# Performance work log

Measured on AMD Instinct MI355X. Metric: run time of the kernel, lower is better.

Reference implementation:

```python
import jax, jax.numpy as jnp
import numpy as np

N = 100_000      # nodes
E = 3_200_000    # edges
F_IN = 9
F_HID = 9
F_OUT = 1
EPS = 1e-5

def _ln(x, g, b):
    m = x.mean(-1, keepdims=True)
    v = x.var(-1, keepdims=True)
    return (x - m) / jnp.sqrt(v + EPS) * g + b

def _gat(x, src, dst, edge_attr, W, a_src, a_dst, We, a_e, bias):
    # Single-head GATConv with edge_dim=1, add_self_loops=True, fill_value='mean'
    n = x.shape[0]
    loop = jnp.arange(n)
    deg = jax.ops.segment_sum(jnp.ones((src.shape[0],), x.dtype), dst, n)
    loop_attr = jax.ops.segment_sum(edge_attr, dst, n) / jnp.maximum(deg, 1.0)[:, None]
    s = jnp.concatenate([src, loop])
    d = jnp.concatenate([dst, loop])
    ea = jnp.concatenate([edge_attr, loop_attr], axis=0)   # [E+N, 1]
    xp = x @ W                                             # [N, C]
    a = (xp * a_src).sum(-1)[s] + (xp * a_dst).sum(-1)[d] + ((ea @ We) * a_e).sum(-1)
    a = jax.nn.leaky_relu(a, 0.2)
    amax = jax.ops.segment_max(a, d, n)
    aexp = jnp.exp(a - amax[d])
    denom = jax.ops.segment_sum(aexp, d, n)
    alpha = aexp / (denom[d] + 1e-16)
    return jax.ops.segment_sum(alpha[:, None] * xp[s], d, n) + bias

def setup_inputs() -> dict:
    key = jax.random.key(0)
    ks = jax.random.split(key, 16)
    def rn(k, shp, s):
        return jax.random.normal(k, shp, jnp.float32) * s
    return {
        "x": jax.random.normal(ks[0], (N, F_IN), jnp.float32),
        "edge_index": jax.random.randint(ks[1], (2, E), 0, N, jnp.int32),
        "edge_attr": jax.random.normal(ks[2], (E, 1), jnp.float32),
        "ln1_g": jnp.ones((F_IN,), jnp.float32), "ln1_b": jnp.zeros((F_IN,), jnp.float32),
        "W0": rn(ks[3], (F_IN, F_HID), 0.3), "as0": rn(ks[4], (F_HID,), 0.3),
        "ad0": rn(ks[5], (F_HID,), 0.3), "We0": rn(ks[6], (1, F_HID), 0.3),
        "ae0": rn(ks[7], (F_HID,), 0.3), "b0": jnp.zeros((F_HID,), jnp.float32),
        "W1": rn(ks[8], (F_HID, F_HID), 0.3), "as1": rn(ks[9], (F_HID,), 0.3),
        "ad1": rn(ks[10], (F_HID,), 0.3), "We1": rn(ks[11], (1, F_HID), 0.3),
        "ae1": rn(ks[12], (F_HID,), 0.3), "b1": jnp.zeros((F_HID,), jnp.float32),
        "ng1": jnp.ones((F_HID,), jnp.float32), "nb1": jnp.zeros((F_HID,), jnp.float32),
        "ln2_g": jnp.ones((2 * F_HID,), jnp.float32), "ln2_b": jnp.zeros((2 * F_HID,), jnp.float32),
        "et_W": rn(ks[13], (2 * F_HID, F_HID), 0.2), "et_b": jnp.zeros((F_HID,), jnp.float32),
        "fc_W": rn(ks[14], (F_HID, F_OUT), 0.3), "fc_b": jnp.zeros((F_OUT,), jnp.float32),
        "att_W": rn(ks[15], (2 * F_OUT, F_OUT), 0.5), "att_b": jnp.zeros((F_OUT,), jnp.float32),
    }

def reference(x, edge_index, edge_attr, ln1_g, ln1_b, W0, as0, ad0, We0, ae0, b0,
              W1, as1, ad1, We1, ae1, b1, ng1, nb1, ln2_g, ln2_b,
              et_W, et_b, fc_W, fc_b, att_W, att_b):
    src, dst = edge_index[0], edge_index[1]
    h = _ln(x, ln1_g, ln1_b)
    # layer 0: no norm/residual
    h = jax.nn.leaky_relu(_gat(h, src, dst, edge_attr, W0, as0, ad0, We0, ae0, b0), 0.01)
    # layer 1: norm + residual
    ident = h
    h = _ln(_gat(h, src, dst, edge_attr, W1, as1, ad1, We1, ae1, b1), ng1, nb1) + ident
    h = jax.nn.leaky_relu(h, 0.01)
    # edge path: gather-concat-norm-MLP  [E, 2H]
    ef = _ln(jnp.concatenate([h[src], h[dst]], axis=1), ln2_g, ln2_b)
    eo = jax.nn.leaky_relu(ef @ et_W + et_b, 0.01)
    eo = eo @ fc_W + fc_b                       # [E, 1]
    # AttentionLayer
    comb = jnp.concatenate([eo, edge_attr], axis=1)   # [E, 2]
    w = jax.nn.softmax(comb @ att_W + att_b, axis=-1) # [E, 1]
    att = (w * comb).sum(axis=1, keepdims=True)       # [E, 1]
    return att + eo
```

## Files before the change

### kernel.cpp

```cpp
#include <hip/hip_runtime.h>
#include <hip/hip_bf16.h>
#include <hip/hip_fp16.h>

typedef __hip_bfloat16 bf16;
typedef unsigned int uint;
typedef unsigned short ushort;
#define TPB 256
#define TPBS 1024
#define TPBG 1024
#define BSH 7
#define BNODES 128
#define NBK_MAX 1024
#define CH 8192
#define EPT (CH / TPBS)
#define NW (TPBS / 64)
#define GPAD 16
#define CAP 4608

enum {
  LN1G = 0, LN1B = 9, PW0 = 18, AS0 = 99, AD0 = 108, CE0 = 117, B0 = 118,
  PW1 = 127, AS1 = 208, AD1 = 217, CE1 = 226, B1 = 227, NG = 236, NB = 245,
  LN2G = 254, LN2B = 272, ETW = 290, ETB = 452, FCW = 461, FCB = 470,
  GC = 471, KC = 480, ETH = 490, NPARAM = 580
};

#ifdef __has_builtin
#if __has_builtin(__builtin_amdgcn_fdot2)
#define HAVE_FDOT2 1
#endif
#endif
#ifndef HAVE_FDOT2
#define HAVE_FDOT2 0
#endif

typedef _Float16 h2f __attribute__((ext_vector_type(2)));

static __device__ __forceinline__ float lrelu(float x, float s) { return x >= 0.f ? x : s * x; }
static __device__ __forceinline__ float ldx(const void* p, long i, int isb) {
    return isb ? __bfloat162float(((const bf16*)p)[i]) : ((const float*)p)[i];
}
static __device__ __forceinline__ uint bfb(float f) {
    uint u = __float_as_uint(f);
    return (u + 0x7FFFu + ((u >> 16) & 1u)) >> 16;
}
static __device__ __forceinline__ uint pack2(float a, float b) { return bfb(a) | (bfb(b) << 16); }
static __device__ __forceinline__ float unlo(uint u) { return __uint_as_float(u << 16); }
static __device__ __forceinline__ float unhi(uint u) { return __uint_as_float(u & 0xFFFF0000u); }
static __device__ __forceinline__ ushort h16(float f) { return __half_as_ushort(__float2half(f)); }
static __device__ __forceinline__ uint p2h(float a, float b) { return (uint)h16(a) | ((uint)h16(b) << 16); }
static __device__ __forceinline__ float hfl(uint u) { return __half2float(__ushort_as_half((ushort)(u & 0xFFFFu))); }
static __device__ __forceinline__ float hfh(uint u) { return __half2float(__ushort_as_half((ushort)(u >> 16))); }
static __device__ __forceinline__ h2f as_h2(uint u) { union { uint u; h2f h; } x; x.u = u; return x.h; }
static __device__ __forceinline__ float dot2f(uint a, uint w, float acc) {
#if HAVE_FDOT2
    return __builtin_amdgcn_fdot2(as_h2(a), as_h2(w), acc, false);
#else
    return fmaf(hfl(a), hfl(w), fmaf(hfh(a), hfh(w), acc));
#endif
}

__global__ void k_params(const void* ln1g, const void* ln1b,
                         const void* W0, const void* as0, const void* ad0,
                         const void* We0, const void* ae0, const void* b0,
                         const void* W1, const void* as1, const void* ad1,
                         const void* We1, const void* ae1, const void* b1,
                         const void* ng, const void* nb,
                         const void* ln2g, const void* ln2b,
                         const void* etW, const void* etb,
                         const void* fcW, const void* fcb,
                         float* __restrict__ P, int* __restrict__ flagp,
                         int* __restrict__ gcursor, int nbk)
{
    __shared__ int sflag;
    if (threadIdx.x == 0) {
        unsigned short h0 = ((const unsigned short*)ln1g)[0];
        sflag = (h0 == 0x3F80u) ? 1 : 0;
        *flagp = sflag;
    }
    __syncthreads();
    const int f = sflag;
    const int t = threadIdx.x;
    for (int j = t; j < nbk; j += TPB) gcursor[j * GPAD] = j * CAP;
    for (int i = t; i < 9; i += TPB) {
        P[LN1G + i] = ldx(ln1g, i, f); P[LN1B + i] = ldx(ln1b, i, f);
        P[AS0 + i] = ldx(as0, i, f);   P[AD0 + i] = ldx(ad0, i, f);
        P[B0 + i]  = ldx(b0, i, f);
        P[AS1 + i] = ldx(as1, i, f);   P[AD1 + i] = ldx(ad1, i, f);
        P[B1 + i]  = ldx(b1, i, f);
        P[NG + i]  = ldx(ng, i, f);    P[NB + i]  = ldx(nb, i, f);
        P[ETB + i] = ldx(etb, i, f);   P[FCW + i] = ldx(fcW, i, f);
    }
    for (int i = t; i < 81; i += TPB) { P[PW0 + i] = ldx(W0, i, f); P[PW1 + i] = ldx(W1, i, f); }
    for (int i = t; i < 18; i += TPB) { P[LN2G + i] = ldx(ln2g, i, f); P[LN2B + i] = ldx(ln2b, i, f); }
    for (int i = t; i < 162; i += TPB) P[ETW + i] = ldx(etW, i, f) * ldx(ln2g, i / 9, f);
    __syncthreads();
    for (int i = t; i < 90; i += TPB) {
        int role = i / 45, rem = i % 45, c = rem / 5, p = rem % 5;
        int k0 = 2 * p, k1 = 2 * p + 1;
        float w0 = (k0 < 9) ? P[ETW + (role * 9 + k0) * 9 + c] : 0.f;
        float w1 = (k1 < 9) ? P[ETW + (role * 9 + k1) * 9 + c] : 0.f;
        ((uint*)P)[ETH + i] = p2h(w0, w1);
    }
    if (t == 0) {
        float c0 = 0.f, c1 = 0.f;
        for (int k = 0; k < 9; k++) {
            c0 += ldx(We0, k, f) * ldx(ae0, k, f);
            c1 += ldx(We1, k, f) * ldx(ae1, k, f);
        }
        P[CE0] = c0; P[CE1] = c1; P[FCB] = ldx(fcb, 0, f);
        for (int c = 0; c < 9; c++) {
            float gc = 0.f, kc = 0.f;
            for (int k = 0; k < 18; k++) {
                float wv = ldx(etW, (long)k * 9 + c, f);
                gc += ldx(ln2g, k, f) * wv;
                kc += ldx(ln2b, k, f) * wv;
            }
            P[GC + c] = gc;
            P[KC + c] = kc + ldx(etb, c, f);
        }
    }
}

__global__ void __launch_bounds__(TPBS)
k_bscatter(const int* __restrict__ src, const int* __restrict__ dst,
           const void* __restrict__ ea, const int* __restrict__ flagp,
           int* __restrict__ gcursor, int2* __restrict__ ebuf, int e, int nbk)
{
    __shared__ int cnt[NBK_MAX];
    __shared__ int cur[NBK_MAX];
    __shared__ int badj[NBK_MAX];
    __shared__ int wsum[NW];
    __shared__ int2 seb[CH];
    const int tid = threadIdx.x;
    const int lane = tid & 63;
    const int wid = tid >> 6;
    const int s0 = blockIdx.x * CH;
    const int m = min(e - s0, CH);
    const int fl = *flagp;
    cnt[tid] = 0;
    __syncthreads();
    int dreg[EPT]; int sreg[EPT]; float ereg[EPT];
    #pragma unroll
    for (int k = 0; k < EPT; k++) {
        int t = tid + k * TPBS;
        if (t < m) {
            dreg[k] = dst[s0 + t];
            sreg[k] = src[s0 + t];
            ereg[k] = ldx(ea, s0 + t, fl);
            atomicAdd(&cnt[dreg[k] >> BSH], 1);
        } else dreg[k] = -1;
    }
    __syncthreads();
    int c = cnt[tid];
    int sc = c;
    #pragma unroll
    for (int o = 1; o < 64; o <<= 1) {
        int v = __shfl_up(sc, o, 64);
        if (lane >= o) sc += v;
    }
    if (lane == 63) wsum[wid] = sc;
    __syncthreads();
    int woff = 0;
    #pragma unroll
    for (int w = 0; w < NW; w++) woff += (w < wid) ? wsum[w] : 0;
    int ex = woff + sc - c;
    cur[tid] = ex;
    int gb = c ? atomicAdd(&gcursor[tid * GPAD], c) : 0;
    badj[tid] = gb - ex;
    __syncthreads();
    #pragma unroll
    for (int k = 0; k < EPT; k++) {
        if (dreg[k] >= 0) {
            int d = dreg[k];
            int b = d >> BSH;
            int slot = atomicAdd(&cur[b], 1);
            seb[slot] = make_int2(sreg[k] | ((d & (BNODES - 1)) << 17),
                                  (int)(bfb(ereg[k]) | ((uint)b << 16)));
        }
    }
    __syncthreads();
    #pragma unroll
    for (int k = 0; k < EPT; k++) {
        int j = tid + k * TPBS;
        if (j < m) {
            int2 v = seb[j];
            int b = (int)((uint)v.y >> 16);
            int pos = badj[b] + j;
            if (pos < (b + 1) * CAP) {
                ebuf[pos] = make_int2(v.x, __float_as_int(unlo((uint)v.y)));
            }
        }
    }
}

__global__ void k_prep(const void* __restrict__ x, const float* __restrict__ P,
                       const int* __restrict__ flagp,
                       uint* __restrict__ xpb0, float* __restrict__ sd0, int n)
{
    const int fl = *flagp;
    int i = blockIdx.x * blockDim.x + threadIdx.x;
    if (i >= n) return;
    float h[9]; float m = 0.f;
    #pragma unroll
    for (int f = 0; f < 9; f++) { h[f] = ldx(x, (long)i * 9 + f, fl); m += h[f]; }
    m *= (1.f / 9.f);
    float v = 0.f;
    #pragma unroll
    for (int f = 0; f < 9; f++) { float d = h[f] - m; v += d * d; }
    float r = rsqrtf(v * (1.f / 9.f) + 1e-5f);
    #pragma unroll
    for (int f = 0; f < 9; f++) h[f] = (h[f] - m) * r * P[LN1G + f] + P[LN1B + f];
    float xr[9]; float ss = 0.f, sd = 0.f;
    #pragma unroll
    for (int c = 0; c < 9; c++) {
        float acc = 0.f;
        #pragma unroll
        for (int f = 0; f < 9; f++) acc += h[f] * P[PW0 + f * 9 + c];
        xr[c] = acc;
        ss += acc * P[AS0 + c]; sd += acc * P[AD0 + c];
    }
    uint* row = xpb0 + (size_t)i * 8;
    ((uint4*)row)[0] = make_uint4(pack2(xr[0], xr[1]), pack2(xr[2], xr[3]),
                                  pack2(xr[4], xr[5]), pack2(xr[6], xr[7]));
    ((uint4*)row)[1] = make_uint4(pack2(xr[8], ss), 0u, 0u, 0u);
    sd0[i] = sd;
}

__global__ void __launch_bounds__(TPBG)
k_sortg0(const int* __restrict__ gcursor, const int2* __restrict__ ebuf,
         const float* __restrict__ P,
         const uint* __restrict__ xpb0, const float* __restrict__ sd0,
         float* __restrict__ h1, uint* __restrict__ xpb1,
         float* __restrict__ sd1, float* __restrict__ la, int n)
{
    __shared__ int2 seb[CAP];
    __shared__ ushort sidx[CAP];
    __shared__ int hist[BNODES], scn[BNODES], cur[BNODES];
    __shared__ int wtot[2];
    const int b = blockIdx.x, tid = threadIdx.x;
    const int beg = b * CAP;
    int cnt = gcursor[b * GPAD] - beg;
    if (cnt > CAP) cnt = CAP;
    if (cnt < 0) cnt = 0;
    if (tid < BNODES) hist[tid] = 0;
    __syncthreads();
    for (int j = tid; j < cnt; j += TPBG) {
        int2 v = ebuf[beg + j];
        seb[j] = v;
        atomicAdd(&hist[(v.x >> 17) & (BNODES - 1)], 1);
    }
    __syncthreads();
    int hc = 0, hsc = 0;
    if (tid < BNODES) {
        hc = hist[tid];
        hsc = hc;
        #pragma unroll
        for (int o = 1; o < 64; o <<= 1) {
            int v = __shfl_up(hsc, o, 64);
            if ((tid & 63) >= o) hsc += v;
        }
        if ((tid & 63) == 63) wtot[tid >> 6] = hsc;
    }
    __syncthreads();
    if (tid < BNODES) {
        int s2 = hsc + ((tid >= 64) ? wtot[0] : 0);
        scn[tid] = s2;
        cur[tid] = s2 - hc;
    }
    __syncthreads();
    for (int j = tid; j < cnt; j += TPBG) {
        int dl = (seb[j].x >> 17) & (BNODES - 1);
        int slot = atomicAdd(&cur[dl], 1);
        sidx[slot] = (ushort)j;
    }
    __syncthreads();
    const int nd = tid >> 3, l = tid & 7;
    const int i = (b << BSH) + nd;
    if (i < n) {
        const float ce = P[CE0];
        const int locend = scn[nd], locbeg = locend - hist[nd];
        const float sdi = sd0[i];
        float acc[11];
        #pragma unroll
        for (int k = 0; k < 11; k++) acc[k] = 0.f;
        for (int j = locbeg + l; j < locend; j += 8) {
            int2 sl = seb[sidx[j]];
            int s = sl.x & 0x1FFFF;
            float eav = __int_as_float(sl.y);
            const uint* row = xpb0 + (size_t)s * 8;
            uint4 q0 = *(const uint4*)row;
            uint  q2 = row[4];
            float ex = expf(lrelu(unhi(q2) + sdi + ce * eav, 0.2f));
            acc[0] += ex; acc[1] += eav;
            acc[2] += ex * unlo(q0.x); acc[3] += ex * unhi(q0.x);
            acc[4] += ex * unlo(q0.y); acc[5] += ex * unhi(q0.y);
            acc[6] += ex * unlo(q0.z); acc[7] += ex * unhi(q0.z);
            acc[8] += ex * unlo(q0.w); acc[9] += ex * unhi(q0.w);
            acc[10] += ex * unlo(q2);
        }
        #pragma unroll
        for (int k = 0; k < 11; k++) {
            acc[k] += __shfl_xor(acc[k], 1, 64);
            acc[k] += __shfl_xor(acc[k], 2, 64);
            acc[k] += __shfl_xor(acc[k], 4, 64);
        }
        if (l == 0) {
            float denom = acc[0];
            float S[9] = {acc[2], acc[3], acc[4], acc[5], acc[6], acc[7], acc[8], acc[9], acc[10]};
            float deg = (float)hist[nd];
            float lav = acc[1] / fmaxf(deg, 1.f);
            la[i] = lav;
            const uint* row = xpb0 + (size_t)i * 8;
            uint4 q0 = *(const uint4*)row;
            uint  q2 = row[4];
            float o0 = unlo(q0.x), o1 = unhi(q0.x), o2 = unlo(q0.y), o3 = unhi(q0.y);
            float o4 = unlo(q0.z), o5 = unhi(q0.z), o6 = unlo(q0.w), o7 = unhi(q0.w);
            float o8 = unlo(q2),   ssi = unhi(q2);
            float ex0 = expf(lrelu(ssi + sdi + ce * lav, 0.2f));
            denom += ex0;
            S[0] += ex0 * o0; S[1] += ex0 * o1; S[2] += ex0 * o2; S[3] += ex0 * o3;
            S[4] += ex0 * o4; S[5] += ex0 * o5; S[6] += ex0 * o6; S[7] += ex0 * o7;
            S[8] += ex0 * o8;
            float inv = 1.f / (denom + 1e-16f);
            float h[9];
            #pragma unroll
            for (int c = 0; c < 9; c++) h[c] = lrelu(S[c] * inv + P[B0 + c], 0.01f);
            float4* hr = (float4*)(h1 + (size_t)i * 12);
            hr[0] = make_float4(h[0], h[1], h[2], h[3]);
            hr[1] = make_float4(h[4], h[5], h[6], h[7]);
            hr[2] = make_float4(h[8], 0.f, 0.f, 0.f);
            float xr1[9]; float ss2 = 0.f, sd2 = 0.f;
            #pragma unroll
            for (int c = 0; c < 9; c++) {
                float a2 = 0.f;
                #pragma unroll
                for (int f = 0; f < 9; f++) a2 += h[f] * P[PW1 + f * 9 + c];
                xr1[c] = a2;
                ss2 += a2 * P[AS1 + c]; sd2 += a2 * P[AD1 + c];
            }
            uint* rw = xpb1 + (size_t)i * 8;
            ((uint4*)rw)[0] = make_uint4(pack2(xr1[0], xr1[1]), pack2(xr1[2], xr1[3]),
                                         pack2(xr1[4], xr1[5]), pack2(xr1[6], xr1[7]));
            ((uint4*)rw)[1] = make_uint4(pack2(xr1[8], ss2), 0u, 0u, 0u);
            sd1[i] = sd2;
        }
    }
}

__global__ void __launch_bounds__(TPBG)
k_sortg1(const int* __restrict__ gcursor, const int2* __restrict__ ebuf,
         const float* __restrict__ P,
         const uint* __restrict__ xpb1, const float* __restrict__ sd1,
         const float* __restrict__ la, const float* __restrict__ h1,
         uint4* __restrict__ orec, int n)
{
    __shared__ int2 seb[CAP];
    __shared__ ushort sidx[CAP];
    __shared__ int hist[BNODES], scn[BNODES], cur[BNODES];
    __shared__ int wtot[2];
    const int b = blockIdx.x, tid = threadIdx.x;
    const int beg = b * CAP;
    int cnt = gcursor[b * GPAD] - beg;
    if (cnt > CAP) cnt = CAP;
    if (cnt < 0) cnt = 0;
    if (tid < BNODES) hist[tid] = 0;
    __syncthreads();
    for (int j = tid; j < cnt; j += TPBG) {
        int2 v = ebuf[beg + j];
        seb[j] = v;
        atomicAdd(&hist[(v.x >> 17) & (BNODES - 1)], 1);
    }
    __syncthreads();
    int hc = 0, hsc = 0;
    if (tid < BNODES) {
        hc = hist[tid];
        hsc = hc;
        #pragma unroll
        for (int o = 1; o < 64; o <<= 1) {
            int v = __shfl_up(hsc, o, 64);
            if ((tid & 63) >= o) hsc += v;
        }
        if ((tid & 63) == 63) wtot[tid >> 6] = hsc;
    }
    __syncthreads();
    if (tid < BNODES) {
        int s2 = hsc + ((tid >= 64) ? wtot[0] : 0);
        scn[tid] = s2;
        cur[tid] = s2 - hc;
    }
    __syncthreads();
    for (int j = tid; j < cnt; j += TPBG) {
        int dl = (seb[j].x >> 17) & (BNODES - 1);
        int slot = atomicAdd(&cur[dl], 1);
        sidx[slot] = (ushort)j;
    }
    __syncthreads();
    const int nd = tid >> 3, l = tid & 7;
    const int i = (b << BSH) + nd;
    if (i < n) {
        const float ce = P[CE1];
        const int locend = scn[nd], locbeg = locend - hist[nd];
        const float sdi = sd1[i];
        float acc[10];
        #pragma unroll
        for (int k = 0; k < 10; k++) acc[k] = 0.f;
        for (int j = locbeg + l; j < locend; j += 8) {
            int2 sl = seb[sidx[j]];
            int s = sl.x & 0x1FFFF;
            float eav = __int_as_float(sl.y);
            const uint* row = xpb1 + (size_t)s * 8;
            uint4 q0 = *(const uint4*)row;
            uint  q2 = row[4];
            float ex = expf(lrelu(unhi(q2) + sdi + ce * eav, 0.2f));
            acc[0] += ex;
            acc[1] += ex * unlo(q0.x); acc[2] += ex * unhi(q0.x);
            acc[3] += ex * unlo(q0.y); acc[4] += ex * unhi(q0.y);
            acc[5] += ex * unlo(q0.z); acc[6] += ex * unhi(q0.z);
            acc[7] += ex * unlo(q0.w); acc[8] += ex * unhi(q0.w);
            acc[9] += ex * unlo(q2);
        }
        #pragma unroll
        for (int k = 0; k < 10; k++) {
            acc[k] += __shfl_xor(acc[k], 1, 64);
            acc[k] += __shfl_xor(acc[k], 2, 64);
            acc[k] += __shfl_xor(acc[k], 4, 64);
        }
        if (l == 0) {
            float denom = acc[0];
            float S[9] = {acc[1], acc[2], acc[3], acc[4], acc[5], acc[6], acc[7], acc[8], acc[9]};
            const uint* row = xpb1 + (size_t)i * 8;
            uint4 q0 = *(const uint4*)row;
            uint  q2 = row[4];
            float o0 = unlo(q0.x), o1 = unhi(q0.x), o2 = unlo(q0.y), o3 = unhi(q0.y);
            float o4 = unlo(q0.z), o5 = unhi(q0.z), o6 = unlo(q0.w), o7 = unhi(q0.w);
            float o8 = unlo(q2),   ssi = unhi(q2);
            float ex0 = expf(lrelu(ssi + sdi + ce * la[i], 0.2f));
            denom += ex0;
            S[0] += ex0 * o0; S[1] += ex0 * o1; S[2] += ex0 * o2; S[3] += ex0 * o3;
            S[4] += ex0 * o4; S[5] += ex0 * o5; S[6] += ex0 * o6; S[7] += ex0 * o7;
            S[8] += ex0 * o8;
            float inv = 1.f / (denom + 1e-16f);
            float g[9]; float m = 0.f;
            #pragma unroll
            for (int c = 0; c < 9; c++) { g[c] = S[c] * inv + P[B1 + c]; m += g[c]; }
            m *= (1.f / 9.f);
            float v = 0.f;
            #pragma unroll
            for (int c = 0; c < 9; c++) { float d = g[c] - m; v += d * d; }
            float r = rsqrtf(v * (1.f / 9.f) + 1e-5f);
            const float4* hr = (const float4*)(h1 + (size_t)i * 12);
            float4 r0 = hr[0], r1 = hr[1], r2 = hr[2];
            float res[9] = {r0.x, r0.y, r0.z, r0.w, r1.x, r1.y, r1.z, r1.w, r2.x};
            float o[9];
            #pragma unroll
            for (int c = 0; c < 9; c++)
                o[c] = lrelu((g[c] - m) * r * P[NG + c] + P[NB + c] + res[c], 0.01f);
            float psum = 0.f, pss = 0.f;
            #pragma unroll
            for (int c = 0; c < 9; c++) { psum += o[c]; pss += o[c] * o[c]; }
            uint4* rp = orec + (size_t)i * 2;
            rp[0] = make_uint4(p2h(o[0], o[1]), p2h(o[2], o[3]), p2h(o[4], o[5]), p2h(o[6], o[7]));
            rp[1] = make_uint4(p2h(o[8], 0.f),
                               __float_as_uint(psum * (1.f / 18.f)),
                               __float_as_uint(pss * (1.f / 18.f)), 0u);
        }
    }
}

__global__ void __launch_bounds__(TPB)
k_edge(const int* __restrict__ src, const int* __restrict__ dst,
       const void* __restrict__ ea, const float* __restrict__ P,
       const int* __restrict__ flagp,
       const uint4* __restrict__ orec, void* __restrict__ outp, int e)
{
    const int fl = *flagp;
    int t = blockIdx.x * blockDim.x + threadIdx.x;
    if (t >= e) return;
    int s = src[t], d = dst[t];
    const uint4* rs = orec + (size_t)s * 2;
    const uint4* rd = orec + (size_t)d * 2;
    uint4 As = rs[0], Bs = rs[1];
    uint4 Ad = rd[0], Bd = rd[1];
    float m   = __uint_as_float(Bs.y) + __uint_as_float(Bd.y);
    float ex2 = __uint_as_float(Bs.z) + __uint_as_float(Bd.z);
    float r = rsqrtf(fmaxf(ex2 - m * m, 0.f) + 1e-5f);
    const uint* eth = (const uint*)P + ETH;
    float eo = P[FCB];
    #pragma unroll
    for (int c = 0; c < 9; c++) {
        float dotc = dot2f(As.x, eth[c * 5 + 0], 0.f);
        dotc = dot2f(As.y, eth[c * 5 + 1], dotc);
        dotc = dot2f(As.z, eth[c * 5 + 2], dotc);
        dotc = dot2f(As.w, eth[c * 5 + 3], dotc);
        dotc = dot2f(Bs.x, eth[c * 5 + 4], dotc);
        dotc = dot2f(Ad.x, eth[45 + c * 5 + 0], dotc);
        dotc = dot2f(Ad.y, eth[45 + c * 5 + 1], dotc);
        dotc = dot2f(Ad.z, eth[45 + c * 5 + 2], dotc);
        dotc = dot2f(Ad.w, eth[45 + c * 5 + 3], dotc);
        dotc = dot2f(Bd.x, eth[45 + c * 5 + 4], dotc);
        float pre = fmaf(r, fmaf(-m, P[GC + c], dotc), P[KC + c]);
        float act = fmaxf(pre, 0.01f * pre);
        eo = fmaf(act, P[FCW + c], eo);
    }
    float resv = 2.f * eo + ldx(ea, t, fl);
    if (fl) ((bf16*)outp)[t] = __float2bfloat16(resv);
    else    ((float*)outp)[t] = resv;
}

extern "C" void kernel_launch(void* const* d_in, const int* in_sizes, int n_in,
                              void* d_out, int out_size, void* d_ws, size_t ws_size,
                              hipStream_t stream) {
    const int n = in_sizes[0] / 9;
    const int e = in_sizes[2];
    const int nbk = (n + BNODES - 1) >> BSH;

    const void* X   = d_in[0];
    const int*  ei  = (const int*)d_in[1];
    const int*  src = ei;
    const int*  dst = ei + e;
    const void* EA  = d_in[2];

    char* base = (char*)d_ws;
    size_t off = 0;
    auto alloc = [&](size_t bytes) { void* p = base + off; off += (bytes + 63) & ~size_t(63); return p; };
    float*  P       = (float*)alloc(1024 * sizeof(float));
    int*    flagp   = (int*)(P + NPARAM);
    int*    gcursor = (int*)alloc((size_t)NBK_MAX * GPAD * sizeof(int));
    int2*   ebuf    = (int2*)alloc((size_t)nbk * CAP * sizeof(int2));
    uint*   xpb0    = (uint*)alloc((size_t)n * 8 * sizeof(uint));
    uint*   xpb1    = (uint*)alloc((size_t)n * 8 * sizeof(uint));
    float*  h1      = (float*)alloc((size_t)n * 12 * sizeof(float));
    uint4*  orec    = (uint4*)alloc((size_t)n * 2 * sizeof(uint4));
    float*  sd0     = (float*)alloc((size_t)n * sizeof(float));
    float*  sd1     = (float*)alloc((size_t)n * sizeof(float));
    float*  la      = (float*)alloc((size_t)n * sizeof(float));

    dim3 gN((n + TPB - 1) / TPB);
    dim3 gE((e + TPB - 1) / TPB);
    dim3 gC((e + CH - 1) / CH);
    dim3 gB(nbk);

    k_params<<<1, TPB, 0, stream>>>(d_in[3], d_in[4], d_in[5], d_in[6], d_in[7],
                                    d_in[8], d_in[9], d_in[10], d_in[11], d_in[12],
                                    d_in[13], d_in[14], d_in[15], d_in[16], d_in[17],
                                    d_in[18], d_in[19], d_in[20], d_in[21], d_in[22],
                                    d_in[23], d_in[24], P, flagp, gcursor, nbk);
    k_prep<<<gN, dim3(TPB), 0, stream>>>(X, P, flagp, xpb0, sd0, n);
    k_bscatter<<<gC, dim3(TPBS), 0, stream>>>(src, dst, EA, flagp, gcursor, ebuf, e, nbk);
    k_sortg0<<<gB, dim3(TPBG), 0, stream>>>(gcursor, ebuf, P, xpb0, sd0, h1, xpb1, sd1, la, n);
    k_sortg1<<<gB, dim3(TPBG), 0, stream>>>(gcursor, ebuf, P, xpb1, sd1, la, h1, orec, n);
    k_edge<<<gE, dim3(TPB), 0, stream>>>(src, dst, EA, P, flagp, orec, d_out, e);
}
```

Before: 175.3 us.

## Persist per-bucket node sort from layer 0 and reuse it in layer 1

The layer-0 gather kernel now writes the locally sorted edge records back to the bucket buffer and stores per-node prefix offsets, so the layer-1 kernel skips its own histogram, scan and local sort and reads the edges directly from global memory. The bucket-scatter kernel is halved to 512 threads, each handling two buckets in the scan and global cursor reservation. The edge MLP kernel processes two edges per thread. This trades an extra write of the edge buffer for removing a whole shared-memory sort pass, while layer 1 now reads edges from global memory instead of LDS.

Result: slower. 182.2 us (+3.9%).

```diff
diff --git a/kernel.cpp b/kernel.cpp
--- a/kernel.cpp
+++ b/kernel.cpp
@@ -6,7 +6,7 @@
 typedef unsigned int uint;
 typedef unsigned short ushort;
 #define TPB 256
-#define TPBS 1024
+#define TPBS 512
 #define TPBG 1024
 #define BSH 7
 #define BNODES 128
@@ -137,7 +137,7 @@
     const int s0 = blockIdx.x * CH;
     const int m = min(e - s0, CH);
     const int fl = *flagp;
-    cnt[tid] = 0;
+    cnt[tid] = 0; cnt[tid + TPBS] = 0;
     __syncthreads();
     int dreg[EPT]; int sreg[EPT]; float ereg[EPT];
     #pragma unroll
@@ -151,8 +151,10 @@
         } else dreg[k] = -1;
     }
     __syncthreads();
-    int c = cnt[tid];
-    int sc = c;
+    const int j0 = tid * 2, j1 = j0 + 1;
+    int c0 = cnt[j0], c1 = cnt[j1];
+    int lsum = c0 + c1;
+    int sc = lsum;
     #pragma unroll
     for (int o = 1; o < 64; o <<= 1) {
         int v = __shfl_up(sc, o, 64);
@@ -163,10 +165,12 @@
     int woff = 0;
     #pragma unroll
     for (int w = 0; w < NW; w++) woff += (w < wid) ? wsum[w] : 0;
-    int ex = woff + sc - c;
-    cur[tid] = ex;
-    int gb = c ? atomicAdd(&gcursor[tid * GPAD], c) : 0;
-    badj[tid] = gb - ex;
+    int e0 = woff + sc - lsum;
+    int e1 = e0 + c0;
+    cur[j0] = e0; cur[j1] = e1;
+    int gb0 = c0 ? atomicAdd(&gcursor[j0 * GPAD], c0) : 0;
+    int gb1 = c1 ? atomicAdd(&gcursor[j1 * GPAD], c1) : 0;
+    badj[j0] = gb0 - e0; badj[j1] = gb1 - e1;
     __syncthreads();
     #pragma unroll
     for (int k = 0; k < EPT; k++) {
@@ -227,11 +231,12 @@
 }
 
 __global__ void __launch_bounds__(TPBG)
-k_sortg0(const int* __restrict__ gcursor, const int2* __restrict__ ebuf,
+k_sortg0(const int* __restrict__ gcursor, int2* __restrict__ ebuf,
          const float* __restrict__ P,
          const uint* __restrict__ xpb0, const float* __restrict__ sd0,
          float* __restrict__ h1, uint* __restrict__ xpb1,
-         float* __restrict__ sd1, float* __restrict__ la, int n)
+         float* __restrict__ sd1, float* __restrict__ la,
+         int* __restrict__ nodeoff, int n)
 {
     __shared__ int2 seb[CAP];
     __shared__ ushort sidx[CAP];
@@ -266,6 +271,7 @@
         int s2 = hsc + ((tid >= 64) ? wtot[0] : 0);
         scn[tid] = s2;
         cur[tid] = s2 - hc;
+        nodeoff[b * BNODES + tid] = s2;
     }
     __syncthreads();
     for (int j = tid; j < cnt; j += TPBG) {
@@ -274,6 +280,7 @@
         sidx[slot] = (ushort)j;
     }
     __syncthreads();
+    for (int j = tid; j < cnt; j += TPBG) ebuf[beg + j] = seb[sidx[j]];
     const int nd = tid >> 3, l = tid & 7;
     const int i = (b << BSH) + nd;
     if (i < n) {
@@ -348,64 +355,29 @@
 }
 
 __global__ void __launch_bounds__(TPBG)
-k_sortg1(const int* __restrict__ gcursor, const int2* __restrict__ ebuf,
+k_sortg1(const int* __restrict__ nodeoff, const int2* __restrict__ ebuf,
          const float* __restrict__ P,
          const uint* __restrict__ xpb1, const float* __restrict__ sd1,
          const float* __restrict__ la, const float* __restrict__ h1,
          uint4* __restrict__ orec, int n)
 {
-    __shared__ int2 seb[CAP];
-    __shared__ ushort sidx[CAP];
-    __shared__ int hist[BNODES], scn[BNODES], cur[BNODES];
-    __shared__ int wtot[2];
+    __shared__ int soff[BNODES];
     const int b = blockIdx.x, tid = threadIdx.x;
     const int beg = b * CAP;
-    int cnt = gcursor[b * GPAD] - beg;
-    if (cnt > CAP) cnt = CAP;
-    if (cnt < 0) cnt = 0;
-    if (tid < BNODES) hist[tid] = 0;
-    __syncthreads();
-    for (int j = tid; j < cnt; j += TPBG) {
-        int2 v = ebuf[beg + j];
-        seb[j] = v;
-        atomicAdd(&hist[(v.x >> 17) & (BNODES - 1)], 1);
-    }
-    __syncthreads();
-    int hc = 0, hsc = 0;
-    if (tid < BNODES) {
-        hc = hist[tid];
-        hsc = hc;
-        #pragma unroll
-        for (int o = 1; o < 64; o <<= 1) {
-            int v = __shfl_up(hsc, o, 64);
-            if ((tid & 63) >= o) hsc += v;
-        }
-        if ((tid & 63) == 63) wtot[tid >> 6] = hsc;
-    }
-    __syncthreads();
-    if (tid < BNODES) {
-        int s2 = hsc + ((tid >= 64) ? wtot[0] : 0);
-        scn[tid] = s2;
-        cur[tid] = s2 - hc;
-    }
-    __syncthreads();
-    for (int j = tid; j < cnt; j += TPBG) {
-        int dl = (seb[j].x >> 17) & (BNODES - 1);
-        int slot = atomicAdd(&cur[dl], 1);
-        sidx[slot] = (ushort)j;
-    }
+    if (tid < BNODES) soff[tid] = nodeoff[b * BNODES + tid];
     __syncthreads();
     const int nd = tid >> 3, l = tid & 7;
     const int i = (b << BSH) + nd;
     if (i < n) {
         const float ce = P[CE1];
-        const int locend = scn[nd], locbeg = locend - hist[nd];
+        const int locbeg = nd ? soff[nd - 1] : 0;
+        const int locend = soff[nd];
         const float sdi = sd1[i];
         float acc[10];
         #pragma unroll
         for (int k = 0; k < 10; k++) acc[k] = 0.f;
         for (int j = locbeg + l; j < locend; j += 8) {
-            int2 sl = seb[sidx[j]];
+            int2 sl = ebuf[beg + j];
             int s = sl.x & 0x1FFFF;
             float eav = __int_as_float(sl.y);
             const uint* row = xpb1 + (size_t)s * 8;
@@ -474,37 +446,42 @@
        const uint4* __restrict__ orec, void* __restrict__ outp, int e)
 {
     const int fl = *flagp;
-    int t = blockIdx.x * blockDim.x + threadIdx.x;
-    if (t >= e) return;
-    int s = src[t], d = dst[t];
-    const uint4* rs = orec + (size_t)s * 2;
-    const uint4* rd = orec + (size_t)d * 2;
-    uint4 As = rs[0], Bs = rs[1];
-    uint4 Ad = rd[0], Bd = rd[1];
-    float m   = __uint_as_float(Bs.y) + __uint_as_float(Bd.y);
-    float ex2 = __uint_as_float(Bs.z) + __uint_as_float(Bd.z);
-    float r = rsqrtf(fmaxf(ex2 - m * m, 0.f) + 1e-5f);
+    const int base = blockIdx.x * (TPB * 2) + threadIdx.x;
     const uint* eth = (const uint*)P + ETH;
-    float eo = P[FCB];
-    #pragma unroll
-    for (int c = 0; c < 9; c++) {
-        float dotc = dot2f(As.x, eth[c * 5 + 0], 0.f);
-        dotc = dot2f(As.y, eth[c * 5 + 1], dotc);
-        dotc = dot2f(As.z, eth[c * 5 + 2], dotc);
-        dotc = dot2f(As.w, eth[c * 5 + 3], dotc);
-        dotc = dot2f(Bs.x, eth[c * 5 + 4], dotc);
-        dotc = dot2f(Ad.x, eth[45 + c * 5 + 0], dotc);
-        dotc = dot2f(Ad.y, eth[45 + c * 5 + 1], dotc);
-        dotc = dot2f(Ad.z, eth[45 + c * 5 + 2], dotc);
-        dotc = dot2f(Ad.w, eth[45 + c * 5 + 3], dotc);
-        dotc = dot2f(Bd.x, eth[45 + c * 5 + 4], dotc);
-        float pre = fmaf(r, fmaf(-m, P[GC + c], dotc), P[KC + c]);
-        float act = fmaxf(pre, 0.01f * pre);
-        eo = fmaf(act, P[FCW + c], eo);
-    }
-    float resv = 2.f * eo + ldx(ea, t, fl);
-    if (fl) ((bf16*)outp)[t] = __float2bfloat16(resv);
-    else    ((float*)outp)[t] = resv;
+    #pragma unroll
+    for (int q = 0; q < 2; q++) {
+        int t = base + q * TPB;
+        if (t < e) {
+            int s = src[t], d = dst[t];
+            const uint4* rs = orec + (size_t)s * 2;
+            const uint4* rd = orec + (size_t)d * 2;
+            uint4 As = rs[0], Bs = rs[1];
+            uint4 Ad = rd[0], Bd = rd[1];
+            float m   = __uint_as_float(Bs.y) + __uint_as_float(Bd.y);
+            float ex2 = __uint_as_float(Bs.z) + __uint_as_float(Bd.z);
+            float r = rsqrtf(fmaxf(ex2 - m * m, 0.f) + 1e-5f);
+            float eo = P[FCB];
+            #pragma unroll
+            for (int c = 0; c < 9; c++) {
+                float dotc = dot2f(As.x, eth[c * 5 + 0], 0.f);
+                dotc = dot2f(As.y, eth[c * 5 + 1], dotc);
+                dotc = dot2f(As.z, eth[c * 5 + 2], dotc);
+                dotc = dot2f(As.w, eth[c * 5 + 3], dotc);
+                dotc = dot2f(Bs.x, eth[c * 5 + 4], dotc);
+                dotc = dot2f(Ad.x, eth[45 + c * 5 + 0], dotc);
+                dotc = dot2f(Ad.y, eth[45 + c * 5 + 1], dotc);
+                dotc = dot2f(Ad.z, eth[45 + c * 5 + 2], dotc);
+                dotc = dot2f(Ad.w, eth[45 + c * 5 + 3], dotc);
+                dotc = dot2f(Bd.x, eth[45 + c * 5 + 4], dotc);
+                float pre = fmaf(r, fmaf(-m, P[GC + c], dotc), P[KC + c]);
+                float act = fmaxf(pre, 0.01f * pre);
+                eo = fmaf(act, P[FCW + c], eo);
+            }
+            float resv = 2.f * eo + ldx(ea, t, fl);
+            if (fl) ((bf16*)outp)[t] = __float2bfloat16(resv);
+            else    ((float*)outp)[t] = resv;
+        }
+    }
 }
 
 extern "C" void kernel_launch(void* const* d_in, const int* in_sizes, int n_in,
@@ -531,12 +508,13 @@
     uint*   xpb1    = (uint*)alloc((size_t)n * 8 * sizeof(uint));
     float*  h1      = (float*)alloc((size_t)n * 12 * sizeof(float));
     uint4*  orec    = (uint4*)alloc((size_t)n * 2 * sizeof(uint4));
+    int*    nodeoff = (int*)alloc((size_t)nbk * BNODES * sizeof(int));
     float*  sd0     = (float*)alloc((size_t)n * sizeof(float));
     float*  sd1     = (float*)alloc((size_t)n * sizeof(float));
     float*  la      = (float*)alloc((size_t)n * sizeof(float));
 
     dim3 gN((n + TPB - 1) / TPB);
-    dim3 gE((e + TPB - 1) / TPB);
+    dim3 gE2((e + TPB * 2 - 1) / (TPB * 2));
     dim3 gC((e + CH - 1) / CH);
     dim3 gB(nbk);
 
@@ -547,7 +525,8 @@
                                     d_in[23], d_in[24], P, flagp, gcursor, nbk);
     k_prep<<<gN, dim3(TPB), 0, stream>>>(X, P, flagp, xpb0, sd0, n);
     k_bscatter<<<gC, dim3(TPBS), 0, stream>>>(src, dst, EA, flagp, gcursor, ebuf, e, nbk);
-    k_sortg0<<<gB, dim3(TPBG), 0, stream>>>(gcursor, ebuf, P, xpb0, sd0, h1, xpb1, sd1, la, n);
-    k_sortg1<<<gB, dim3(TPBG), 0, stream>>>(gcursor, ebuf, P, xpb1, sd1, la, h1, orec, n);
-    k_edge<<<gE, dim3(TPB), 0, stream>>>(src, dst, EA, P, flagp, orec, d_out, e);
-}
+    k_sortg0<<<gB, dim3(TPBG), 0, stream>>>(gcursor, ebuf, P, xpb0, sd0, h1, xpb1, sd1, la,
+                                            nodeoff, n);
+    k_sortg1<<<gB, dim3(TPBG), 0, stream>>>(nodeoff, ebuf, P, xpb1, sd1, la, h1, orec, n);
+    k_edge<<<gE2, dim3(TPB), 0, stream>>>(src, dst, EA, P, flagp, orec, d_out, e);
+}
```
